# Optimization experiments

Measured on AMD Instinct MI355X. Metric: run time of the kernel, lower is better.

The kernel has to match this reference:

```python
import jax, jax.numpy as jnp
import numpy as np
from jax.scipy.special import logsumexp

B, D, T, O = 8, 64, 512, 256  # batch, channels (d_dim), observed timestamps, grid points


def setup_inputs() -> dict:
    key = jax.random.key(0)
    k1, k2, k3 = jax.random.split(key, 3)
    vals = jax.random.normal(k1, (B, D, T), dtype=jnp.float32)
    mask = (jax.random.uniform(k2, (B, D, T)) < 0.7).astype(jnp.float32)
    mask = mask.at[:, :, 0].set(1.0)  # ensure >=1 observation per (b, channel)
    times = jnp.sort(jax.random.uniform(k3, (B, D, T), dtype=jnp.float32), axis=-1)
    x = jnp.concatenate([vals, mask, times], axis=1)  # (B, 3*D, T)
    grid = jnp.broadcast_to(jnp.linspace(0.0, 1.0, O, dtype=jnp.float32), (B, O))
    kernel = jnp.zeros((D,), dtype=jnp.float32)  # learned per-channel log-bandwidth
    return {"x": x, "interpolation_grid": grid, "kernel": kernel}


def reference(x, interpolation_grid, kernel):
    d_dim = kernel.shape[0]
    x_t = x[:, :d_dim]            # (B, D, T) observed values
    m = x[:, d_dim:2 * d_dim]     # (B, D, T) observation mask in {0,1}
    t = x[:, 2 * d_dim:3 * d_dim] # (B, D, T) observation timestamps

    alpha = jax.nn.softplus(kernel)[None, :, None, None]  # pos_kernel, (1,D,1,1)
    # squared distance between observed times and reference grid: (B,D,T,O)
    norm = (t[:, :, :, None] - interpolation_grid[:, None, None, :]) ** 2
    # log(mask): -inf (clamped) where unobserved, 0 where observed
    logm = jnp.log(jnp.maximum(m, 1e-30))[:, :, :, None]

    s = -alpha * norm + logm                      # (B,D,T,O) masked RBF logits
    w = logsumexp(s, axis=2)                      # (B,D,O) intensity channel
    w1 = jnp.exp(s - w[:, :, None, :])            # softmax over T
    y = jnp.sum(w1 * x_t[:, :, :, None], axis=2)  # (B,D,O) smooth interpolation

    s10 = -10.0 * alpha * norm + logm             # sharper kernel (transient)
    wt_lse = logsumexp(s10, axis=2)
    wt = jnp.exp(s10 - wt_lse[:, :, None, :])
    y_trans = jnp.sum(wt * x_t[:, :, :, None], axis=2)  # (B,D,O)

    return jnp.concatenate([y, w, y_trans], axis=1)  # (B, 3*D, O)
```

## Files before the change

### kernel.cpp

```cpp
#include <hip/hip_runtime.h>
#include <math.h>


namespace {
constexpr int kB = 8, kD = 64, kT = 512, kO = 256;
constexpr int kTH = 512;
constexpr float kLOG2E = 1.4426950408889634f;
constexpr float kLN2   = 0.6931471805599453f;
constexpr float kLM    = 99.65784284662087f;
}

__device__ __forceinline__ float2 pkfma(float2 a, float b, float2 c) {
    return make_float2(fmaf(a.x, b, c.x), fmaf(a.y, b, c.y));
}
__device__ __forceinline__ float2 pkadd(float2 a, float2 b) {
    return make_float2(a.x + b.x, a.y + b.y);
}

__global__ __launch_bounds__(kTH, 4) void interp_kernel(
    const float* __restrict__ x,
    const float* __restrict__ grid,
    const float* __restrict__ kern,
    float* __restrict__ out)
{
    __shared__ __align__(16) float smem[4096 + 8];
    float* s_u   = smem;
    float* s_w   = smem + kT;
    float* s_v   = smem + 2 * kT;
    float* s_cnt = smem + 4096;

    const int tid  = threadIdx.x;
    const int lane = tid & 63;
    const int wv   = tid >> 6;
    const int ow   = wv & 1;
    const int tq   = wv >> 1;
    const int o0   = ow * 128 + lane;
    const int o1   = o0 + 64;

    const int bd = blockIdx.x;
    const int b  = bd >> 6;
    const int d  = bd & (kD - 1);

    const float* base = x + (size_t)b * (3 * kD * kT);
    const float* Vrow = base + (size_t)d * kT;
    const float* Mrow = base + (size_t)(kD + d) * kT;
    const float* Trow = base + (size_t)(2 * kD + d) * kT;

    const float k     = kern[d];
    const float alpha = fmaxf(k, 0.0f) + log1pf(expf(-fabsf(k)));
    const float a2    = alpha * kLOG2E;

    const float tt = Trow[tid];
    const float mm = Mrow[tid];
    const float vv = Vrow[tid];
    const bool keep = (mm != 0.0f);
    const unsigned long long ball = __ballot(keep);
    if (lane == 0) s_cnt[wv] = (float)__popcll(ball);
    __syncthreads();

    int bsum = 0, total = 0;
    #pragma unroll
    for (int j = 0; j < 8; ++j) {
        const int c = (int)s_cnt[j];
        bsum  += (j < wv) ? c : 0;
        total += c;
    }
    const int padded = (total + 15) & ~15;

    if (keep) {
        const int pos = bsum + __popcll(ball & ((1ull << lane) - 1ull));
        s_u[pos] = fmaf(-a2 * tt, tt, 0.0f);
        s_w[pos] = 2.0f * a2 * tt;
        s_v[pos] = vv;
    }
    if (tid >= total && tid < padded) {
        s_u[tid] = -500.0f;
        s_w[tid] = 0.0f;
        s_v[tid] = 0.0f;
    }
    __syncthreads();

    const float g0 = grid[b * kO + o0];
    const float g1 = grid[b * kO + o1];
    const float2 cc = make_float2(-a2 * g0 * g0, -a2 * g1 * g1);

    float2 acc_l = make_float2(0.f, 0.f), acc_y = make_float2(0.f, 0.f);
    float2 acc_q = make_float2(0.f, 0.f), acc_z = make_float2(0.f, 0.f);

    const int chunk = padded >> 2;
    const int t0 = tq * chunk;
    for (int t = t0; t < t0 + chunk; t += 4) {
        const float4 uu = *(const float4*)(s_u + t);
        const float4 ww = *(const float4*)(s_w + t);
        const float4 vs = *(const float4*)(s_v + t);

        #pragma unroll
        for (int j = 0; j < 4; ++j) {
            const float u = (&uu.x)[j], w = (&ww.x)[j], v = (&vs.x)[j];
            const float2 a = pkadd(pkfma(make_float2(g0, g1), w,
                                         make_float2(u, u)), cc);
            const float2 e = make_float2(__builtin_amdgcn_exp2f(a.x),
                                         __builtin_amdgcn_exp2f(a.y));
            const float2 E = make_float2(__builtin_amdgcn_exp2f(10.0f * a.x),
                                         __builtin_amdgcn_exp2f(10.0f * a.y));
            acc_l = pkadd(acc_l, e);
            acc_y = pkfma(e, v, acc_y);
            acc_q = pkadd(acc_q, E);
            acc_z = pkfma(E, v, acc_z);
        }
    }

    __syncthreads();
    float (*sp)[4][kO] = (float (*)[4][kO])smem;
    sp[tq][0][o0] = acc_l.x;  sp[tq][0][o1] = acc_l.y;
    sp[tq][1][o0] = acc_y.x;  sp[tq][1][o1] = acc_y.y;
    sp[tq][2][o0] = acc_q.x;  sp[tq][2][o1] = acc_q.y;
    sp[tq][3][o0] = acc_z.x;  sp[tq][3][o1] = acc_z.y;
    __syncthreads();

    if (tq == 0) {
        float L0=0.f,L1=0.f, Y0=0.f,Y1=0.f, Q0=0.f,Q1=0.f, Z0=0.f,Z1=0.f;
        #pragma unroll
        for (int j = 0; j < 4; ++j) {
            L0 += sp[j][0][o0]; Y0 += sp[j][1][o0];
            Q0 += sp[j][2][o0]; Z0 += sp[j][3][o0];
            L1 += sp[j][0][o1]; Y1 += sp[j][1][o1];
            Q1 += sp[j][2][o1]; Z1 += sp[j][3][o1];
        }
        const float w0o = __builtin_amdgcn_logf(L0) * kLN2;
        const float w1o = __builtin_amdgcn_logf(L1) * kLN2;
        float* ob = out + (size_t)b * (3 * kD * kO);
        ob[(size_t)d * kO + o0]            = Y0 / L0;
        ob[(size_t)d * kO + o1]            = Y1 / L1;
        ob[(size_t)(kD + d) * kO + o0]     = w0o;
        ob[(size_t)(kD + d) * kO + o1]     = w1o;
        ob[(size_t)(2 * kD + d) * kO + o0] = Z0 / Q0;
        ob[(size_t)(2 * kD + d) * kO + o1] = Z1 / Q1;
    }
}

extern "C" void kernel_launch(void* const* d_in, const int* in_sizes, int n_in,
                              void* d_out, int out_size, void* d_ws, size_t ws_size,
                              hipStream_t stream) {
    const float* x    = (const float*)d_in[0];
    const float* grid = (const float*)d_in[1];
    const float* kern = (const float*)d_in[2];
    float* out        = (float*)d_out;
    interp_kernel<<<dim3(kB * kD), dim3(kTH), 0, stream>>>(x, grid, kern, out);
}
```

Before: 72.48 us.

## Give each wave all 256 grid points and split observations across eight waves

Each wave now covers all 256 grid outputs (four per lane) over one eighth of the compacted observations, instead of 128 outputs over one quarter. Each LDS load of u/w/v now feeds four output points instead of two, which cuts LDS traffic per exp. The reduction now sums eight partial sets, with the block split in two halves: one writes y and the log-sum, the other writes y_trans. Shared memory doubles to 32KB, the launch-bounds occupancy hint rises to 8, and more accumulators per thread raise register pressure.

```diff
diff --git a/kernel.cpp b/kernel.cpp
--- a/kernel.cpp
+++ b/kernel.cpp
@@ -7,7 +7,6 @@
 constexpr int kTH = 512;
 constexpr float kLOG2E = 1.4426950408889634f;
 constexpr float kLN2   = 0.6931471805599453f;
-constexpr float kLM    = 99.65784284662087f;
 }
 
 __device__ __forceinline__ float2 pkfma(float2 a, float b, float2 c) {
@@ -17,25 +16,25 @@
     return make_float2(a.x + b.x, a.y + b.y);
 }
 
-__global__ __launch_bounds__(kTH, 4) void interp_kernel(
+__global__ __launch_bounds__(kTH, 8) void interp_kernel(
     const float* __restrict__ x,
     const float* __restrict__ grid,
     const float* __restrict__ kern,
     float* __restrict__ out)
 {
-    __shared__ __align__(16) float smem[4096 + 8];
+    __shared__ __align__(16) float smem[8192 + 8];
     float* s_u   = smem;
     float* s_w   = smem + kT;
     float* s_v   = smem + 2 * kT;
-    float* s_cnt = smem + 4096;
+    float* s_cnt = smem + 8192;
 
     const int tid  = threadIdx.x;
     const int lane = tid & 63;
     const int wv   = tid >> 6;
-    const int ow   = wv & 1;
-    const int tq   = wv >> 1;
-    const int o0   = ow * 128 + lane;
-    const int o1   = o0 + 64;
+    const int o0   = lane;
+    const int o1   = lane + 64;
+    const int o2   = lane + 128;
+    const int o3   = lane + 192;
 
     const int bd = blockIdx.x;
     const int b  = bd >> 6;
@@ -65,11 +64,11 @@
         bsum  += (j < wv) ? c : 0;
         total += c;
     }
-    const int padded = (total + 15) & ~15;
+    const int padded = (total + 31) & ~31;
 
     if (keep) {
         const int pos = bsum + __popcll(ball & ((1ull << lane) - 1ull));
-        s_u[pos] = fmaf(-a2 * tt, tt, 0.0f);
+        s_u[pos] = -a2 * tt * tt;
         s_w[pos] = 2.0f * a2 * tt;
         s_v[pos] = vv;
     }
@@ -80,15 +79,19 @@
     }
     __syncthreads();
 
-    const float g0 = grid[b * kO + o0];
-    const float g1 = grid[b * kO + o1];
-    const float2 cc = make_float2(-a2 * g0 * g0, -a2 * g1 * g1);
+    const int gb = b * kO;
+    const float2 g01 = make_float2(grid[gb + o0], grid[gb + o1]);
+    const float2 g23 = make_float2(grid[gb + o2], grid[gb + o3]);
+    const float2 c01 = make_float2(-a2 * g01.x * g01.x, -a2 * g01.y * g01.y);
+    const float2 c23 = make_float2(-a2 * g23.x * g23.x, -a2 * g23.y * g23.y);
 
-    float2 acc_l = make_float2(0.f, 0.f), acc_y = make_float2(0.f, 0.f);
-    float2 acc_q = make_float2(0.f, 0.f), acc_z = make_float2(0.f, 0.f);
+    float2 l01 = make_float2(0.f, 0.f), l23 = make_float2(0.f, 0.f);
+    float2 y01 = make_float2(0.f, 0.f), y23 = make_float2(0.f, 0.f);
+    float2 q01 = make_float2(0.f, 0.f), q23 = make_float2(0.f, 0.f);
+    float2 z01 = make_float2(0.f, 0.f), z23 = make_float2(0.f, 0.f);
 
-    const int chunk = padded >> 2;
-    const int t0 = tq * chunk;
+    const int chunk = padded >> 3;
+    const int t0 = wv * chunk;
     for (int t = t0; t < t0 + chunk; t += 4) {
         const float4 uu = *(const float4*)(s_u + t);
         const float4 ww = *(const float4*)(s_w + t);
@@ -97,45 +100,49 @@
         #pragma unroll
         for (int j = 0; j < 4; ++j) {
             const float u = (&uu.x)[j], w = (&ww.x)[j], v = (&vs.x)[j];
-            const float2 a = pkadd(pkfma(make_float2(g0, g1), w,
-                                         make_float2(u, u)), cc);
-            const float2 e = make_float2(__builtin_amdgcn_exp2f(a.x),
-                                         __builtin_amdgcn_exp2f(a.y));
-            const float2 E = make_float2(__builtin_amdgcn_exp2f(10.0f * a.x),
-                                         __builtin_amdgcn_exp2f(10.0f * a.y));
-            acc_l = pkadd(acc_l, e);
-            acc_y = pkfma(e, v, acc_y);
-            acc_q = pkadd(acc_q, E);
-            acc_z = pkfma(E, v, acc_z);
+            const float2 a01v = pkadd(pkfma(g01, w, make_float2(u, u)), c01);
+            const float2 a23v = pkadd(pkfma(g23, w, make_float2(u, u)), c23);
+            const float2 e01 = make_float2(__builtin_amdgcn_exp2f(a01v.x),
+                                           __builtin_amdgcn_exp2f(a01v.y));
+            const float2 e23 = make_float2(__builtin_amdgcn_exp2f(a23v.x),
+                                           __builtin_amdgcn_exp2f(a23v.y));
+            const float2 E01 = make_float2(__builtin_amdgcn_exp2f(10.0f * a01v.x),
+                                           __builtin_amdgcn_exp2f(10.0f * a01v.y));
+            const float2 E23 = make_float2(__builtin_amdgcn_exp2f(10.0f * a23v.x),
+                                           __builtin_amdgcn_exp2f(10.0f * a23v.y));
+            l01 = pkadd(l01, e01);  l23 = pkadd(l23, e23);
+            y01 = pkfma(e01, v, y01);  y23 = pkfma(e23, v, y23);
+            q01 = pkadd(q01, E01);  q23 = pkadd(q23, E23);
+            z01 = pkfma(E01, v, z01);  z23 = pkfma(E23, v, z23);
         }
     }
 
     __syncthreads();
     float (*sp)[4][kO] = (float (*)[4][kO])smem;
-    sp[tq][0][o0] = acc_l.x;  sp[tq][0][o1] = acc_l.y;
-    sp[tq][1][o0] = acc_y.x;  sp[tq][1][o1] = acc_y.y;
-    sp[tq][2][o0] = acc_q.x;  sp[tq][2][o1] = acc_q.y;
-    sp[tq][3][o0] = acc_z.x;  sp[tq][3][o1] = acc_z.y;
+    sp[wv][0][o0] = l01.x; sp[wv][0][o1] = l01.y;
+    sp[wv][0][o2] = l23.x; sp[wv][0][o3] = l23.y;
+    sp[wv][1][o0] = y01.x; sp[wv][1][o1] = y01.y;
+    sp[wv][1][o2] = y23.x; sp[wv][1][o3] = y23.y;
+    sp[wv][2][o0] = q01.x; sp[wv][2][o1] = q01.y;
+    sp[wv][2][o2] = q23.x; sp[wv][2][o3] = q23.y;
+    sp[wv][3][o0] = z01.x; sp[wv][3][o1] = z01.y;
+    sp[wv][3][o2] = z23.x; sp[wv][3][o3] = z23.y;
     __syncthreads();
 
-    if (tq == 0) {
-        float L0=0.f,L1=0.f, Y0=0.f,Y1=0.f, Q0=0.f,Q1=0.f, Z0=0.f,Z1=0.f;
+    float* ob = out + (size_t)b * (3 * kD * kO);
+    if (tid < kO) {
+        const int o = tid;
+        float L = 0.f, Y = 0.f;
         #pragma unroll
-        for (int j = 0; j < 4; ++j) {
-            L0 += sp[j][0][o0]; Y0 += sp[j][1][o0];
-            Q0 += sp[j][2][o0]; Z0 += sp[j][3][o0];
-            L1 += sp[j][0][o1]; Y1 += sp[j][1][o1];
-            Q1 += sp[j][2][o1]; Z1 += sp[j][3][o1];
-        }
-        const float w0o = __builtin_amdgcn_logf(L0) * kLN2;
-        const float w1o = __builtin_amdgcn_logf(L1) * kLN2;
-        float* ob = out + (size_t)b * (3 * kD * kO);
-        ob[(size_t)d * kO + o0]            = Y0 / L0;
-        ob[(size_t)d * kO + o1]            = Y1 / L1;
-        ob[(size_t)(kD + d) * kO + o0]     = w0o;
-        ob[(size_t)(kD + d) * kO + o1]     = w1o;
-        ob[(size_t)(2 * kD + d) * kO + o0] = Z0 / Q0;
-        ob[(size_t)(2 * kD + d) * kO + o1] = Z1 / Q1;
+        for (int j = 0; j < 8; ++j) { L += sp[j][0][o]; Y += sp[j][1][o]; }
+        ob[(size_t)d * kO + o]        = Y / L;
+        ob[(size_t)(kD + d) * kO + o] = __builtin_amdgcn_logf(L) * kLN2;
+    } else {
+        const int o = tid - kO;
+        float Q = 0.f, Z = 0.f;
+        #pragma unroll
+        for (int j = 0; j < 8; ++j) { Q += sp[j][2][o]; Z += sp[j][3][o]; }
+        ob[(size_t)(2 * kD + d) * kO + o] = Z / Q;
     }
 }
 
```

New measurement: 72.62 us. No clear change (+0.2%).
